# Optimization experiments

Measured on AMD Instinct MI355X. Metric: run time of the kernel, lower is better.

Reference implementation:

```python
import jax, jax.numpy as jnp
import numpy as np

B, N, E = 128, 256, 2048
BINS = 16

def _gcn(x, src, dst, W, b):
    # GCNConv with self-loops and symmetric deg^-1/2 normalization (PyG default).
    h = x @ W  # [N, Fout]
    deg = jnp.zeros(x.shape[0], x.dtype).at[dst].add(1.0) + 1.0  # +1 self-loop
    dinv = jax.lax.rsqrt(deg)
    coef = dinv[src] * dinv[dst]  # [E]
    agg = jnp.zeros_like(h).at[dst].add(h[src] * coef[:, None])
    return agg + h / deg[:, None] + b  # self-loop norm = 1/deg

def _gnn(x, ei, W1, b1, W2, b2, W3, b3):
    # x: [B,N,Fin], ei: [B,2,E]. Dropout skipped (eval mode).
    def single(x, ei):
        s, d = ei[0], ei[1]
        h = jax.nn.relu(_gcn(x, s, d, W1, b1))
        h = jax.nn.relu(_gcn(h, s, d, W2, b2))
        return _gcn(h, s, d, W3, b3)
    return jax.vmap(single)(x, ei)

def _att_pool(x, Watt):
    # SimGNN attention pooling; all graphs have exactly N nodes.
    ctx = jnp.tanh((x @ Watt.T).sum(axis=1) / jnp.asarray(N, x.dtype))  # [B,f3]
    scores = jax.nn.sigmoid(jnp.einsum('bnf,bf->bn', x, ctx))  # [B,N]
    return jnp.einsum('bnf,bn->bf', x, scores)  # [B,f3]

def _forward(xq, xc, eq, ec, W1, b1, W2, b2, W3, b3, Watt, ntnW, ntnV, ntnb, fc1W, fc1b, fc2W, fc2b):
    q = _gnn(xq, eq, W1, b1, W2, b2, W3, b3)  # [B,N,f3]
    c = _gnn(xc, ec, W1, b1, W2, b2, W3, b3)
    e1 = _att_pool(q, Watt)
    e2 = _att_pool(c, Watt)
    # NTN: bilinear + linear on concat + bias
    scores = jax.nn.relu(
        jnp.einsum('bi,tij,bj->bt', e1, ntnW, e2)
        + jnp.concatenate([e1, e2], axis=-1) @ ntnV.T
        + ntnb
    )  # [B, tensor_neurons]
    # histogram of all pairwise node-embedding dot products (torch.histc semantics)
    s = jnp.einsum('bnf,bmf->bnm', q, c).ravel()
    lo, hi = s.min(), s.max()
    idx = jnp.clip(jnp.floor((s - lo) / (hi - lo) * BINS).astype(jnp.int32), 0, BINS - 1)
    counts = jnp.zeros(BINS, s.dtype).at[idx].add(1.0)
    h = jax.lax.stop_gradient(counts / counts.sum())
    scores = jnp.concatenate([scores, jnp.broadcast_to(h, (scores.shape[0], BINS))], axis=1)
    scores = jax.nn.relu(scores @ fc1W.T + fc1b)
    p = jax.nn.sigmoid(scores @ fc2W.T + fc2b)  # [B,1]
    return p.squeeze()


def setup_inputs() -> dict:
    key = jax.random.key(0)
    ks = jax.random.split(key, 20)
    Fin, f1, f2, f3, T, BN = 128, 128, 64, 32, 16, 16
    def xav(k, shape):
        fan_in, fan_out = shape[-1], shape[0]
        lim = np.sqrt(6.0 / (fan_in + fan_out))
        return jax.random.uniform(k, shape, jnp.float32, -lim, lim)
    return {
        'xq': jax.random.normal(ks[0], (B, N, Fin), jnp.float32),
        'xc': jax.random.normal(ks[1], (B, N, Fin), jnp.float32),
        'eq': jax.random.randint(ks[2], (B, 2, E), 0, N, jnp.int32),
        'ec': jax.random.randint(ks[3], (B, 2, E), 0, N, jnp.int32),
        'W1': xav(ks[4], (Fin, f1)), 'b1': jnp.zeros((f1,), jnp.float32),
        'W2': xav(ks[5], (f1, f2)), 'b2': jnp.zeros((f2,), jnp.float32),
        'W3': xav(ks[6], (f2, f3)), 'b3': jnp.zeros((f3,), jnp.float32),
        'Watt': xav(ks[7], (f3, f3)),
        'ntnW': xav(ks[8], (T, f3, f3)),
        'ntnV': xav(ks[9], (T, 2 * f3)),
        'ntnb': xav(ks[10], (T, 1)).squeeze(-1),
        'fc1W': xav(ks[11], (BN, T + BINS)), 'fc1b': jnp.zeros((BN,), jnp.float32),
        'fc2W': xav(ks[12], (1, BN)), 'fc2b': jnp.zeros((1,), jnp.float32),
    }


def reference(xq, xc, eq, ec, W1, b1, W2, b2, W3, b3, Watt, ntnW, ntnV, ntnb, fc1W, fc1b, fc2W, fc2b):
    return _forward(xq, xc, eq, ec, W1, b1, W2, b2, W3, b3, Watt, ntnW, ntnV, ntnb, fc1W, fc1b, fc2W, fc2b)
```

## Files before the change

### kernel.cpp

```cpp
#include <hip/hip_runtime.h>
#include <math.h>

#define BB 128
#define NN 256
#define EE 2048
#define BINS 16
#define HTS 36

typedef unsigned short u16;

__global__ void csr_kernel(const int* __restrict__ eq, const int* __restrict__ ec,
                           int* __restrict__ off, u16* __restrict__ srcs,
                           float* __restrict__ dvsg) {
    int g = blockIdx.x;
    int b = g < BB ? g : g - BB;
    const int* ei = g < BB ? eq : ec;
    int t = threadIdx.x;
    __shared__ int cnt[NN];
    __shared__ int sa[NN], sb[NN];
    __shared__ int cursor[NN];
    cnt[t] = 0;
    __syncthreads();
    const int* src = ei + b * 2 * EE;
    const int* dst = src + EE;
    for (int e = t; e < EE; e += 256) atomicAdd(&cnt[dst[e]], 1);
    __syncthreads();
    dvsg[g * NN + t] = rsqrtf((float)cnt[t] + 1.0f);
    sa[t] = cnt[t];
    __syncthreads();
    int* pin = sa; int* pout = sb;
    for (int d = 1; d < NN; d <<= 1) {
        int v = pin[t];
        if (t >= d) v += pin[t - d];
        pout[t] = v;
        __syncthreads();
        int* tmp = pin; pin = pout; pout = tmp;
    }
    int excl = pin[t] - cnt[t];
    off[g * 257 + t] = excl;
    if (t == 255) off[g * 257 + 256] = EE;
    cursor[t] = excl;
    __syncthreads();
    for (int e = t; e < EE; e += 256) {
        int d = dst[e], s = src[e];
        int pos = atomicAdd(&cursor[d], 1);
        srcs[g * EE + pos] = (u16)s;
    }
}

template<int FIN, int FOUT, bool RELU, int NSPLIT>
__global__ __launch_bounds__(256, 3) void gcn_fused3(
        const float* __restrict__ X0, const float* __restrict__ X1,
        const float* __restrict__ W, const float* __restrict__ bias,
        const int* __restrict__ off, const u16* __restrict__ srcs,
        const float* __restrict__ dvsg, float* __restrict__ OUT) {
    constexpr int CHUNKS = FOUT / 32;
    int blk = blockIdx.x;
    int g = blk % (2 * BB);
    int rest = blk / (2 * BB);
    int cb = (rest % CHUNKS) * 32;
    int half = rest / CHUNKS;
    int t = threadIdx.x;

    __shared__ float hT[NN * HTS];
    __shared__ float xsT[8 * 260];
    __shared__ float wt[8 * 32];
    __shared__ int   eoff[NN + 1];
    __shared__ u16   esrc[EE];
    __shared__ float dvs_s[NN];

    const float* xg = (g < BB) ? (X0 + (size_t)g * NN * FIN)
                               : (X1 + (size_t)(g - BB) * NN * FIN);
    const int* o = off + g * 257;
    const u16* sr = srcs + (size_t)g * EE;

    for (int i = t; i < EE; i += 256) esrc[i] = sr[i];
    for (int i = t; i <= NN; i += 256) eoff[i] = o[i];
    dvs_s[t] = dvsg[g * NN + t];

    int l = t & 63;
    int wv = t >> 6;

    float acc[4][8];
#pragma unroll
    for (int i = 0; i < 4; i++)
#pragma unroll
        for (int j = 0; j < 8; j++) acc[i][j] = 0.f;

    const float* xr = xg + t * FIN;
    float4 va = *(const float4*)(xr);
    float4 vb = *(const float4*)(xr + 4);
    int wrow = t >> 5, wcol = t & 31;
    float wreg = W[wrow * FOUT + cb + wcol];

    for (int k0 = 0; k0 < FIN; k0 += 8) {
        xsT[0 * 260 + t] = va.x;
        xsT[1 * 260 + t] = va.y;
        xsT[2 * 260 + t] = va.z;
        xsT[3 * 260 + t] = va.w;
        xsT[4 * 260 + t] = vb.x;
        xsT[5 * 260 + t] = vb.y;
        xsT[6 * 260 + t] = vb.z;
        xsT[7 * 260 + t] = vb.w;
        wt[t] = wreg;
        __syncthreads();
        if (k0 + 8 < FIN) {
            va = *(const float4*)(xr + k0 + 8);
            vb = *(const float4*)(xr + k0 + 12);
            wreg = W[(k0 + 8 + wrow) * FOUT + cb + wcol];
        }
#pragma unroll
        for (int k = 0; k < 8; k++) {
            float4 xv = *(const float4*)&xsT[k * 260 + 4 * l];
            float4 wa = *(const float4*)&wt[k * 32 + 8 * wv];
            float4 wb = *(const float4*)&wt[k * 32 + 8 * wv + 4];
            float xq4[4] = {xv.x, xv.y, xv.z, xv.w};
            float wc8[8] = {wa.x, wa.y, wa.z, wa.w, wb.x, wb.y, wb.z, wb.w};
#pragma unroll
            for (int i = 0; i < 4; i++)
#pragma unroll
                for (int j = 0; j < 8; j++) acc[i][j] += xq4[i] * wc8[j];
        }
        __syncthreads();
    }
#pragma unroll
    for (int i = 0; i < 4; i++) {
        *(float4*)&hT[(4 * l + i) * HTS + 8 * wv] =
            make_float4(acc[i][0], acc[i][1], acc[i][2], acc[i][3]);
        *(float4*)&hT[(4 * l + i) * HTS + 8 * wv + 4] =
            make_float4(acc[i][4], acc[i][5], acc[i][6], acc[i][7]);
    }
    __syncthreads();

    int c = t & 31, ng = t >> 5;
    float bb_ = bias[cb + c];
    float* outp = OUT + (size_t)g * NN * FOUT;
    constexpr int NSEG = NN / NSPLIT;
    int nlo = half * NSEG, nhi = nlo + NSEG;
    for (int n = nlo + ng; n < nhi; n += 8) {
        int j0 = eoff[n], j1 = eoff[n + 1];
        float dn = dvs_s[n];
        float a = 0.f;
        int j = j0;
        for (; j + 1 < j1; j += 2) {
            int s0 = esrc[j], s1 = esrc[j + 1];
            float w0 = dvs_s[s0] * dn, w1 = dvs_s[s1] * dn;
            a += hT[s0 * HTS + c] * w0;
            a += hT[s1 * HTS + c] * w1;
        }
        if (j < j1) {
            int s0 = esrc[j];
            a += hT[s0 * HTS + c] * (dvs_s[s0] * dn);
        }
        float d0i = 1.0f / ((float)(j1 - j0) + 1.0f);
        float val = a + hT[n * HTS + c] * d0i + bb_;
        if (RELU) val = fmaxf(val, 0.f);
        outp[n * FOUT + cb + c] = val;
    }
}

__global__ void attpool_kernel(const float* __restrict__ X, const float* __restrict__ Watt,
                               float* __restrict__ e) {
    int g = blockIdx.x;
    int t = threadIdx.x;
    __shared__ float xs[NN * 33];
    __shared__ float red[256];
    __shared__ float mean_s[32], ctx_s[32], sc[NN];
    const float* x = X + (size_t)g * NN * 32;
    for (int i = t; i < NN * 32; i += 256) { int n = i >> 5, c = i & 31; xs[n * 33 + c] = x[i]; }
    __syncthreads();
    {
        int c = t & 31, p = t >> 5;
        float s = 0.f;
        for (int n = p * 32; n < (p + 1) * 32; n++) s += xs[n * 33 + c];
        red[t] = s;
    }
    __syncthreads();
    if (t < 32) {
        float m = 0.f;
        for (int p = 0; p < 8; p++) m += red[p * 32 + t];
        mean_s[t] = m / (float)NN;
    }
    __syncthreads();
    if (t < 32) {
        float a = 0.f;
        for (int f = 0; f < 32; f++) a += mean_s[f] * Watt[t * 32 + f];
        ctx_s[t] = tanhf(a);
    }
    __syncthreads();
    {
        float a = 0.f;
        for (int f = 0; f < 32; f++) a += xs[t * 33 + f] * ctx_s[f];
        sc[t] = 1.f / (1.f + expf(-a));
    }
    __syncthreads();
    {
        int c = t & 31, p = t >> 5;
        float s = 0.f;
        for (int n = p * 32; n < (p + 1) * 32; n++) s += xs[n * 33 + c] * sc[n];
        red[t] = s;
    }
    __syncthreads();
    if (t < 32) {
        float s = 0.f;
        for (int p = 0; p < 8; p++) s += red[p * 32 + t];
        e[g * 32 + t] = s;
    }
}

#define PD_STAGE_AND_DOT \
    int blk = blockIdx.x; \
    int b = blk >> 2; \
    int tq = (blk >> 1) & 1, tc = blk & 1; \
    __shared__ float qsT[32 * 132]; \
    __shared__ float csT[32 * 132]; \
    int t = threadIdx.x; \
    { \
        int n = t >> 1, f0 = (t & 1) * 16; \
        const float* qp = Q + ((size_t)b * NN + tq * 128 + n) * 32 + f0; \
        const float* cp = C + ((size_t)b * NN + tc * 128 + n) * 32 + f0; \
        float qa16[16], ca16[16]; \
        *(float4*)&qa16[0]  = *(const float4*)(qp); \
        *(float4*)&qa16[4]  = *(const float4*)(qp + 4); \
        *(float4*)&qa16[8]  = *(const float4*)(qp + 8); \
        *(float4*)&qa16[12] = *(const float4*)(qp + 12); \
        *(float4*)&ca16[0]  = *(const float4*)(cp); \
        *(float4*)&ca16[4]  = *(const float4*)(cp + 4); \
        *(float4*)&ca16[8]  = *(const float4*)(cp + 8); \
        *(float4*)&ca16[12] = *(const float4*)(cp + 12); \
        _Pragma("unroll") \
        for (int m = 0; m < 16; m++) { \
            qsT[(f0 + m) * 132 + n] = qa16[m]; \
            csT[(f0 + m) * 132 + n] = ca16[m]; \
        } \
    } \
    __syncthreads(); \
    int rg = (t >> 4) * 4, cg = (t & 15) * 4; \
    float acc[8][8]; \
    _Pragma("unroll") \
    for (int i = 0; i < 8; i++) \
        _Pragma("unroll") \
        for (int j = 0; j < 8; j++) acc[i][j] = 0.f; \
    _Pragma("unroll 2") \
    for (int f = 0; f < 32; f++) { \
        float4 qa = *(const float4*)&qsT[f * 132 + rg]; \
        float4 qb = *(const float4*)&qsT[f * 132 + 64 + rg]; \
        float4 ca = *(const float4*)&csT[f * 132 + cg]; \
        float4 cb = *(const float4*)&csT[f * 132 + 64 + cg]; \
        float qv[8] = {qa.x, qa.y, qa.z, qa.w, qb.x, qb.y, qb.z, qb.w}; \
        float cv[8] = {ca.x, ca.y, ca.z, ca.w, cb.x, cb.y, cb.z, cb.w}; \
        _Pragma("unroll") \
        for (int i = 0; i < 8; i++) \
            _Pragma("unroll") \
            for (int j = 0; j < 8; j++) acc[i][j] += qv[i] * cv[j]; \
    }

__global__ __launch_bounds__(256, 4) void pairdot_minmax(
        const float* __restrict__ Q, const float* __restrict__ C,
        float* __restrict__ bmin, float* __restrict__ bmax) {
    PD_STAGE_AND_DOT
    float lmin = acc[0][0], lmax = acc[0][0];
#pragma unroll
    for (int i = 0; i < 8; i++)
#pragma unroll
        for (int j = 0; j < 8; j++) {
            lmin = fminf(lmin, acc[i][j]);
            lmax = fmaxf(lmax, acc[i][j]);
        }
    __shared__ float rmin[256], rmax[256];
    rmin[t] = lmin; rmax[t] = lmax;
    __syncthreads();
    for (int s = 128; s > 0; s >>= 1) {
        if (t < s) { rmin[t] = fminf(rmin[t], rmin[t + s]); rmax[t] = fmaxf(rmax[t], rmax[t + s]); }
        __syncthreads();
    }
    if (t == 0) { bmin[blk] = rmin[0]; bmax[blk] = rmax[0]; }
}

__global__ void minmax_kernel(const float* __restrict__ bmin, const float* __restrict__ bmax,
                              float* __restrict__ lohi, float* __restrict__ counts) {
    __shared__ float rmin[256], rmax[256];
    int t = threadIdx.x;
    float lmin = 1e30f, lmax = -1e30f;
    for (int i = t; i < 512; i += 256) { lmin = fminf(lmin, bmin[i]); lmax = fmaxf(lmax, bmax[i]); }
    rmin[t] = lmin; rmax[t] = lmax;
    __syncthreads();
    for (int s = 128; s > 0; s >>= 1) {
        if (t < s) { rmin[t] = fminf(rmin[t], rmin[t + s]); rmax[t] = fmaxf(rmax[t], rmax[t + s]); }
        __syncthreads();
    }
    if (t == 0) { lohi[0] = rmin[0]; lohi[1] = rmax[0]; }
    if (t < BINS) counts[t] = 0.f;
}

__global__ __launch_bounds__(256, 4) void pairdot_hist(
        const float* __restrict__ Q, const float* __restrict__ C,
        const float* __restrict__ lohi, float* __restrict__ counts) {
    PD_STAGE_AND_DOT
    float lo = lohi[0], hi = lohi[1];
    float scale = (float)BINS / (hi - lo);
    int lane = t & 63;
    int cnt = 0;
#pragma unroll
    for (int i = 0; i < 8; i++)
#pragma unroll
        for (int j = 0; j < 8; j++) {
            int idx = (int)floorf((acc[i][j] - lo) * scale);
            idx = min(max(idx, 0), BINS - 1);
            unsigned long long b0 = __ballot((idx & 1) != 0);
            unsigned long long b1 = __ballot((idx & 2) != 0);
            unsigned long long b2 = __ballot((idx & 4) != 0);
            unsigned long long b3 = __ballot((idx & 8) != 0);
            unsigned long long msk = ((lane & 1) ? b0 : ~b0);
            msk &= ((lane & 2) ? b1 : ~b1);
            msk &= ((lane & 4) ? b2 : ~b2);
            msk &= ((lane & 8) ? b3 : ~b3);
            cnt += __popcll(msk);
        }
    __shared__ float wbins[4][BINS];
    int wave = t >> 6;
    if (lane < BINS) wbins[wave][lane] = (float)cnt;
    __syncthreads();
    if (t < BINS) {
        atomicAdd(&counts[t], wbins[0][t] + wbins[1][t] + wbins[2][t] + wbins[3][t]);
    }
}

__global__ void final_kernel(const float* __restrict__ e1, const float* __restrict__ e2,
                             const float* __restrict__ ntnW, const float* __restrict__ ntnV,
                             const float* __restrict__ ntnb, const float* __restrict__ counts,
                             const float* __restrict__ fc1W, const float* __restrict__ fc1b,
                             const float* __restrict__ fc2W, const float* __restrict__ fc2b,
                             float* __restrict__ out) {
    int b = blockIdx.x;
    int t = threadIdx.x;
    __shared__ float a1[32], a2[32], red[256], z[32], u[16];
    if (t < 32) a1[t] = e1[b * 32 + t];
    else if (t < 64) a2[t - 32] = e2[b * 32 + t - 32];
    __syncthreads();
    int tt = t >> 4, g = t & 15;
    float p = 0.f;
#pragma unroll
    for (int ii = 0; ii < 2; ii++) {
        int i = g + 16 * ii;
        float d = 0.f;
        const float* wr = ntnW + (tt * 32 + i) * 32;
        for (int j = 0; j < 32; j++) d += wr[j] * a2[j];
        p += a1[i] * d;
    }
    red[t] = p;
    __syncthreads();
    if (t < 16) {
        float s = 0.f;
        for (int g2 = 0; g2 < 16; g2++) s += red[t * 16 + g2];
        float lin = ntnb[t];
        for (int i = 0; i < 32; i++) lin += ntnV[t * 64 + i] * a1[i];
        for (int i = 0; i < 32; i++) lin += ntnV[t * 64 + 32 + i] * a2[i];
        z[t] = fmaxf(s + lin, 0.f);
    } else if (t < 32) {
        float tot = 0.f;
        for (int i = 0; i < BINS; i++) tot += counts[i];
        z[t] = counts[t - 16] / tot;
    }
    __syncthreads();
    if (t < 16) {
        float a = fc1b[t];
        for (int i = 0; i < 32; i++) a += fc1W[t * 32 + i] * z[i];
        u[t] = fmaxf(a, 0.f);
    }
    __syncthreads();
    if (t == 0) {
        float a = fc2b[0];
        for (int i = 0; i < 16; i++) a += fc2W[i] * u[i];
        out[b] = 1.f / (1.f + expf(-a));
    }
}

extern "C" void kernel_launch(void* const* d_in, const int* in_sizes, int n_in,
                              void* d_out, int out_size, void* d_ws, size_t ws_size,
                              hipStream_t stream) {
    const float* xq   = (const float*)d_in[0];
    const float* xc   = (const float*)d_in[1];
    const int*   eq   = (const int*)d_in[2];
    const int*   ec   = (const int*)d_in[3];
    const float* W1   = (const float*)d_in[4];
    const float* b1   = (const float*)d_in[5];
    const float* W2   = (const float*)d_in[6];
    const float* b2   = (const float*)d_in[7];
    const float* W3   = (const float*)d_in[8];
    const float* b3   = (const float*)d_in[9];
    const float* Watt = (const float*)d_in[10];
    const float* ntnW = (const float*)d_in[11];
    const float* ntnV = (const float*)d_in[12];
    const float* ntnb = (const float*)d_in[13];
    const float* fc1W = (const float*)d_in[14];
    const float* fc1b = (const float*)d_in[15];
    const float* fc2W = (const float*)d_in[16];
    const float* fc2b = (const float*)d_in[17];
    float* out = (float*)d_out;
    float* ws  = (float*)d_ws;

    float* O3   = ws;
    float* e12  = O3 + 2097152;
    float* bmin = e12 + 8192;
    float* bmax = bmin + 2048;
    float* lohi = bmax + 2048;
    float* cntw = lohi + 2;
    int*   off  = (int*)(ws + 2109504);
    u16*   srcs = (u16*)(off + 65792);
    float* dvsg = ws + 2109504 + 65792 + 524288;
    float* O1   = ws + 3223872;
    float* O2   = O1 + 8388608;

    float* O3Q = O3;
    float* O3C = O3 + (size_t)BB * NN * 32;
    float* e1w = e12;
    float* e2w = e12 + BB * 32;

    csr_kernel<<<2 * BB, 256, 0, stream>>>(eq, ec, off, srcs, dvsg);

    gcn_fused3<128, 128, true, 1><<<4 * 2 * BB, 256, 0, stream>>>(
        xq, xc, W1, b1, off, srcs, dvsg, O1);
    gcn_fused3<128, 64, true, 1><<<2 * 2 * BB, 256, 0, stream>>>(
        O1, O1 + (size_t)BB * NN * 128, W2, b2, off, srcs, dvsg, O2);
    gcn_fused3<64, 32, false, 2><<<2 * 2 * BB, 256, 0, stream>>>(
        O2, O2 + (size_t)BB * NN * 64, W3, b3, off, srcs, dvsg, O3);

    attpool_kernel<<<2 * BB, 256, 0, stream>>>(O3, Watt, e12);

    pairdot_minmax<<<BB * 4, 256, 0, stream>>>(O3Q, O3C, bmin, bmax);
    minmax_kernel<<<1, 256, 0, stream>>>(bmin, bmax, lohi, cntw);
    pairdot_hist<<<BB * 4, 256, 0, stream>>>(O3Q, O3C, lohi, cntw);

    final_kernel<<<BB, 256, 0, stream>>>(e1w, e2w, ntnW, ntnV, ntnb, cntw,
                                         fc1W, fc1b, fc2W, fc2b, out);
}
```

Measured before the change: 327.9 us.

## Split fused GCN layers into separate row-tiled GEMM and gather kernels

Each fused per-graph GCN kernel, which recomputed the GEMM per 32-column chunk with a small 8-wide K tile, is replaced by a standalone row-tiled GEMM kernel writing H to a workspace buffer, followed by a gather kernel that aggregates neighbours from H staged in shared memory. Layer 1 is split into two 64-column halves so one temporary buffer can be reused, and O2 aliases O1 to shrink the workspace. The goal is better GEMM tiling (K=16, full-width output tiles, higher occupancy) and less redundant X reading. The cost is extra global round trips of H and twice as many kernel launches.

```diff
diff --git a/kernel.cpp b/kernel.cpp
--- a/kernel.cpp
+++ b/kernel.cpp
@@ -5,7 +5,6 @@
 #define NN 256
 #define EE 2048
 #define BINS 16
-#define HTS 36
 
 typedef unsigned short u16;
 
@@ -48,114 +47,137 @@
     }
 }
 
-template<int FIN, int FOUT, bool RELU, int NSPLIT>
-__global__ __launch_bounds__(256, 3) void gcn_fused3(
+template<int FIN, int FOUT, int WLD>
+__global__ __launch_bounds__(256, 4) void gemm_k(
         const float* __restrict__ X0, const float* __restrict__ X1,
-        const float* __restrict__ W, const float* __restrict__ bias,
+        const float* __restrict__ W, float* __restrict__ H) {
+    constexpr int NCG = FOUT / 4;
+    constexpr int NRG = 256 / NCG;
+    constexpr int TILE_R = NRG * 4;
+    constexpr int XSTR = TILE_R + 4;
+    constexpr int NF4 = TILE_R / 64;
+    __shared__ float xsT[16 * XSTR];
+    __shared__ float wt[16 * FOUT];
+    int t = threadIdx.x;
+    size_t row0 = (size_t)blockIdx.x * TILE_R;
+
+    const float* xp[NF4];
+#pragma unroll
+    for (int i = 0; i < NF4; i++) {
+        int f = t + 256 * i;
+        int r = f >> 2;
+        size_t gr = row0 + r;
+        const float* base = (gr < (size_t)BB * NN)
+                            ? X0 + gr * FIN
+                            : X1 + (gr - (size_t)BB * NN) * FIN;
+        xp[i] = base + (f & 3) * 4;
+    }
+    float4 xa[NF4];
+#pragma unroll
+    for (int i = 0; i < NF4; i++) xa[i] = *(const float4*)xp[i];
+
+    int wrow, wcol; bool wact;
+    if (FOUT == 64) { wrow = t >> 4; wcol = (t & 15) * 4; wact = true; }
+    else            { wrow = t >> 3; wcol = (t & 7) * 4;  wact = (t < 128); }
+    float4 wa4 = make_float4(0.f, 0.f, 0.f, 0.f);
+    if (wact) wa4 = *(const float4*)&W[(size_t)wrow * WLD + wcol];
+
+    int colg = t & (NCG - 1); int cg = colg * 4;
+    int rowg = t / NCG;       int rg = rowg * 4;
+
+    float acc[4][4];
+#pragma unroll
+    for (int i = 0; i < 4; i++)
+#pragma unroll
+        for (int j = 0; j < 4; j++) acc[i][j] = 0.f;
+
+    for (int k0 = 0; k0 < FIN; k0 += 16) {
+#pragma unroll
+        for (int i = 0; i < NF4; i++) {
+            int f = t + 256 * i;
+            int r = f >> 2;
+            int kq = (f & 3) * 4;
+            xsT[(kq + 0) * XSTR + r] = xa[i].x;
+            xsT[(kq + 1) * XSTR + r] = xa[i].y;
+            xsT[(kq + 2) * XSTR + r] = xa[i].z;
+            xsT[(kq + 3) * XSTR + r] = xa[i].w;
+        }
+        if (wact) *(float4*)&wt[wrow * FOUT + wcol] = wa4;
+        __syncthreads();
+        if (k0 + 16 < FIN) {
+#pragma unroll
+            for (int i = 0; i < NF4; i++) xa[i] = *(const float4*)(xp[i] + k0 + 16);
+            if (wact) wa4 = *(const float4*)&W[(size_t)(k0 + 16 + wrow) * WLD + wcol];
+        }
+#pragma unroll
+        for (int k = 0; k < 16; k++) {
+            float4 xv = *(const float4*)&xsT[k * XSTR + rg];
+            float4 wv = *(const float4*)&wt[k * FOUT + cg];
+            acc[0][0] += xv.x * wv.x; acc[0][1] += xv.x * wv.y;
+            acc[0][2] += xv.x * wv.z; acc[0][3] += xv.x * wv.w;
+            acc[1][0] += xv.y * wv.x; acc[1][1] += xv.y * wv.y;
+            acc[1][2] += xv.y * wv.z; acc[1][3] += xv.y * wv.w;
+            acc[2][0] += xv.z * wv.x; acc[2][1] += xv.z * wv.y;
+            acc[2][2] += xv.z * wv.z; acc[2][3] += xv.z * wv.w;
+            acc[3][0] += xv.w * wv.x; acc[3][1] += xv.w * wv.y;
+            acc[3][2] += xv.w * wv.z; acc[3][3] += xv.w * wv.w;
+        }
+        __syncthreads();
+    }
+#pragma unroll
+    for (int i = 0; i < 4; i++) {
+        *(float4*)&H[(row0 + rg + i) * FOUT + cg] =
+            make_float4(acc[i][0], acc[i][1], acc[i][2], acc[i][3]);
+    }
+}
+
+template<int FH, int OLD, bool RELU>
+__global__ __launch_bounds__(256, 4) void gather_k(
+        const float* __restrict__ H, const float* __restrict__ bias,
         const int* __restrict__ off, const u16* __restrict__ srcs,
         const float* __restrict__ dvsg, float* __restrict__ OUT) {
-    constexpr int CHUNKS = FOUT / 32;
+    constexpr int NCH = FH / 32;
     int blk = blockIdx.x;
-    int g = blk % (2 * BB);
-    int rest = blk / (2 * BB);
-    int cb = (rest % CHUNKS) * 32;
-    int half = rest / CHUNKS;
-    int t = threadIdx.x;
-
-    __shared__ float hT[NN * HTS];
-    __shared__ float xsT[8 * 260];
-    __shared__ float wt[8 * 32];
+    int g = blk / NCH, ch = blk % NCH;
+    int cb = ch * 32;
+    __shared__ float hT[NN * 33];
     __shared__ int   eoff[NN + 1];
     __shared__ u16   esrc[EE];
     __shared__ float dvs_s[NN];
-
-    const float* xg = (g < BB) ? (X0 + (size_t)g * NN * FIN)
-                               : (X1 + (size_t)(g - BB) * NN * FIN);
+    int t = threadIdx.x;
+    const float* Hg = H + (size_t)g * NN * FH + cb;
+#pragma unroll
+    for (int i = 0; i < 8; i++) {
+        int idx = t + 256 * i;
+        int n = idx >> 3, c4 = (idx & 7) * 4;
+        float4 v = *(const float4*)&Hg[(size_t)n * FH + c4];
+        hT[n * 33 + c4 + 0] = v.x;
+        hT[n * 33 + c4 + 1] = v.y;
+        hT[n * 33 + c4 + 2] = v.z;
+        hT[n * 33 + c4 + 3] = v.w;
+    }
+    const u16* sr = srcs + (size_t)g * EE;
+    for (int i = t; i < EE; i += 256) esrc[i] = sr[i];
     const int* o = off + g * 257;
-    const u16* sr = srcs + (size_t)g * EE;
-
-    for (int i = t; i < EE; i += 256) esrc[i] = sr[i];
     for (int i = t; i <= NN; i += 256) eoff[i] = o[i];
     dvs_s[t] = dvsg[g * NN + t];
-
-    int l = t & 63;
-    int wv = t >> 6;
-
-    float acc[4][8];
-#pragma unroll
-    for (int i = 0; i < 4; i++)
-#pragma unroll
-        for (int j = 0; j < 8; j++) acc[i][j] = 0.f;
-
-    const float* xr = xg + t * FIN;
-    float4 va = *(const float4*)(xr);
-    float4 vb = *(const float4*)(xr + 4);
-    int wrow = t >> 5, wcol = t & 31;
-    float wreg = W[wrow * FOUT + cb + wcol];
-
-    for (int k0 = 0; k0 < FIN; k0 += 8) {
-        xsT[0 * 260 + t] = va.x;
-        xsT[1 * 260 + t] = va.y;
-        xsT[2 * 260 + t] = va.z;
-        xsT[3 * 260 + t] = va.w;
-        xsT[4 * 260 + t] = vb.x;
-        xsT[5 * 260 + t] = vb.y;
-        xsT[6 * 260 + t] = vb.z;
-        xsT[7 * 260 + t] = vb.w;
-        wt[t] = wreg;
-        __syncthreads();
-        if (k0 + 8 < FIN) {
-            va = *(const float4*)(xr + k0 + 8);
-            vb = *(const float4*)(xr + k0 + 12);
-            wreg = W[(k0 + 8 + wrow) * FOUT + cb + wcol];
-        }
-#pragma unroll
-        for (int k = 0; k < 8; k++) {
-            float4 xv = *(const float4*)&xsT[k * 260 + 4 * l];
-            float4 wa = *(const float4*)&wt[k * 32 + 8 * wv];
-            float4 wb = *(const float4*)&wt[k * 32 + 8 * wv + 4];
-            float xq4[4] = {xv.x, xv.y, xv.z, xv.w};
-            float wc8[8] = {wa.x, wa.y, wa.z, wa.w, wb.x, wb.y, wb.z, wb.w};
-#pragma unroll
-            for (int i = 0; i < 4; i++)
-#pragma unroll
-                for (int j = 0; j < 8; j++) acc[i][j] += xq4[i] * wc8[j];
-        }
-        __syncthreads();
-    }
-#pragma unroll
-    for (int i = 0; i < 4; i++) {
-        *(float4*)&hT[(4 * l + i) * HTS + 8 * wv] =
-            make_float4(acc[i][0], acc[i][1], acc[i][2], acc[i][3]);
-        *(float4*)&hT[(4 * l + i) * HTS + 8 * wv + 4] =
-            make_float4(acc[i][4], acc[i][5], acc[i][6], acc[i][7]);
-    }
     __syncthreads();
 
     int c = t & 31, ng = t >> 5;
     float bb_ = bias[cb + c];
-    float* outp = OUT + (size_t)g * NN * FOUT;
-    constexpr int NSEG = NN / NSPLIT;
-    int nlo = half * NSEG, nhi = nlo + NSEG;
-    for (int n = nlo + ng; n < nhi; n += 8) {
+    float* outp = OUT + (size_t)g * NN * OLD + cb + c;
+    for (int n = ng; n < NN; n += 8) {
         int j0 = eoff[n], j1 = eoff[n + 1];
         float dn = dvs_s[n];
         float a = 0.f;
-        int j = j0;
-        for (; j + 1 < j1; j += 2) {
-            int s0 = esrc[j], s1 = esrc[j + 1];
-            float w0 = dvs_s[s0] * dn, w1 = dvs_s[s1] * dn;
-            a += hT[s0 * HTS + c] * w0;
-            a += hT[s1 * HTS + c] * w1;
-        }
-        if (j < j1) {
-            int s0 = esrc[j];
-            a += hT[s0 * HTS + c] * (dvs_s[s0] * dn);
+        for (int j = j0; j < j1; j++) {
+            int s = esrc[j];
+            a += hT[s * 33 + c] * (dvs_s[s] * dn);
         }
         float d0i = 1.0f / ((float)(j1 - j0) + 1.0f);
-        float val = a + hT[n * HTS + c] * d0i + bb_;
+        float val = a + hT[n * 33 + c] * d0i + bb_;
         if (RELU) val = fmaxf(val, 0.f);
-        outp[n * FOUT + cb + c] = val;
+        outp[(size_t)n * OLD] = val;
     }
 }
 
@@ -408,9 +430,10 @@
     float* cntw = lohi + 2;
     int*   off  = (int*)(ws + 2109504);
     u16*   srcs = (u16*)(off + 65792);
-    float* dvsg = ws + 2109504 + 65792 + 524288;
-    float* O1   = ws + 3223872;
-    float* O2   = O1 + 8388608;
+    float* dvsg = ws + 2437440;
+    float* Htmp = ws + 2502976;
+    float* O1   = ws + 6697280;
+    float* O2   = O1;
 
     float* O3Q = O3;
     float* O3C = O3 + (size_t)BB * NN * 32;
@@ -419,12 +442,16 @@
 
     csr_kernel<<<2 * BB, 256, 0, stream>>>(eq, ec, off, srcs, dvsg);
 
-    gcn_fused3<128, 128, true, 1><<<4 * 2 * BB, 256, 0, stream>>>(
-        xq, xc, W1, b1, off, srcs, dvsg, O1);
-    gcn_fused3<128, 64, true, 1><<<2 * 2 * BB, 256, 0, stream>>>(
-        O1, O1 + (size_t)BB * NN * 128, W2, b2, off, srcs, dvsg, O2);
-    gcn_fused3<64, 32, false, 2><<<2 * 2 * BB, 256, 0, stream>>>(
-        O2, O2 + (size_t)BB * NN * 64, W3, b3, off, srcs, dvsg, O3);
+    gemm_k<128, 64, 128><<<1024, 256, 0, stream>>>(xq, xc, W1, Htmp);
+    gather_k<64, 128, true><<<512, 256, 0, stream>>>(Htmp, b1, off, srcs, dvsg, O1);
+    gemm_k<128, 64, 128><<<1024, 256, 0, stream>>>(xq, xc, W1 + 64, Htmp);
+    gather_k<64, 128, true><<<512, 256, 0, stream>>>(Htmp, b1 + 64, off, srcs, dvsg, O1 + 64);
+
+    gemm_k<128, 64, 64><<<1024, 256, 0, stream>>>(O1, O1 + (size_t)BB * NN * 128, W2, Htmp);
+    gather_k<64, 64, true><<<512, 256, 0, stream>>>(Htmp, b2, off, srcs, dvsg, O2);
+
+    gemm_k<64, 32, 32><<<512, 256, 0, stream>>>(O2, O2 + (size_t)BB * NN * 64, W3, Htmp);
+    gather_k<32, 32, false><<<256, 256, 0, stream>>>(Htmp, b3, off, srcs, dvsg, O3);
 
     attpool_kernel<<<2 * BB, 256, 0, stream>>>(O3, Watt, e12);
 
```

Result: slower. 547.8 us (+67.1%).

## Widen GCN blocks to 512 threads with aliased shared buffer and smaller tiles

Applied to the files above, without the earlier changes.

The fused GCN kernel now runs 512 threads per block, and each thread computes a 4x4 output tile instead of 4x8. The k-step grows from 8 to 16, and the aggregation loop strides over 16 node groups. The staging buffers for X and W share one shared-memory array with the h tile, which shrinks LDS use so more blocks can be resident. The intent is higher occupancy and fewer register-heavy accumulators, traded against less register reuse per FMA and the change in LDS padding from 36 to 33, which drops float4 stores and may cause bank conflicts.

```diff
diff --git a/kernel.cpp b/kernel.cpp
--- a/kernel.cpp
+++ b/kernel.cpp
@@ -5,7 +5,6 @@
 #define NN 256
 #define EE 2048
 #define BINS 16
-#define HTS 36
 
 typedef unsigned short u16;
 
@@ -49,7 +48,7 @@
 }
 
 template<int FIN, int FOUT, bool RELU, int NSPLIT>
-__global__ __launch_bounds__(256, 3) void gcn_fused3(
+__global__ __launch_bounds__(512, 8) void gcn_fused4(
         const float* __restrict__ X0, const float* __restrict__ X1,
         const float* __restrict__ W, const float* __restrict__ bias,
         const int* __restrict__ off, const u16* __restrict__ srcs,
@@ -62,74 +61,75 @@
     int half = rest / CHUNKS;
     int t = threadIdx.x;
 
-    __shared__ float hT[NN * HTS];
-    __shared__ float xsT[8 * 260];
-    __shared__ float wt[8 * 32];
+    __shared__ float uni[NN * 33];
     __shared__ int   eoff[NN + 1];
     __shared__ u16   esrc[EE];
     __shared__ float dvs_s[NN];
+    float* xsT = uni;
+    float* wt  = uni + 16 * 260;
+    float* hT  = uni;
 
     const float* xg = (g < BB) ? (X0 + (size_t)g * NN * FIN)
                                : (X1 + (size_t)(g - BB) * NN * FIN);
     const int* o = off + g * 257;
     const u16* sr = srcs + (size_t)g * EE;
 
-    for (int i = t; i < EE; i += 256) esrc[i] = sr[i];
-    for (int i = t; i <= NN; i += 256) eoff[i] = o[i];
-    dvs_s[t] = dvsg[g * NN + t];
+    for (int i = t; i < EE; i += 512) esrc[i] = sr[i];
+    for (int i = t; i <= NN; i += 512) eoff[i] = o[i];
+    if (t < NN) dvs_s[t] = dvsg[g * NN + t];
 
     int l = t & 63;
     int wv = t >> 6;
 
-    float acc[4][8];
+    float acc[4][4];
 #pragma unroll
     for (int i = 0; i < 4; i++)
 #pragma unroll
-        for (int j = 0; j < 8; j++) acc[i][j] = 0.f;
-
-    const float* xr = xg + t * FIN;
-    float4 va = *(const float4*)(xr);
-    float4 vb = *(const float4*)(xr + 4);
-    int wrow = t >> 5, wcol = t & 31;
-    float wreg = W[wrow * FOUT + cb + wcol];
-
-    for (int k0 = 0; k0 < FIN; k0 += 8) {
-        xsT[0 * 260 + t] = va.x;
-        xsT[1 * 260 + t] = va.y;
-        xsT[2 * 260 + t] = va.z;
-        xsT[3 * 260 + t] = va.w;
-        xsT[4 * 260 + t] = vb.x;
-        xsT[5 * 260 + t] = vb.y;
-        xsT[6 * 260 + t] = vb.z;
-        xsT[7 * 260 + t] = vb.w;
+        for (int j = 0; j < 4; j++) acc[i][j] = 0.f;
+
+    int sn = t >> 1, qk = (t & 1) * 8;
+    const float* xr = xg + sn * FIN + qk;
+    float4 v0 = *(const float4*)xr;
+    float4 v1 = *(const float4*)(xr + 4);
+    float wreg = W[(t >> 5) * FOUT + cb + (t & 31)];
+
+    for (int k0 = 0; k0 < FIN; k0 += 16) {
+        xsT[(qk + 0) * 260 + sn] = v0.x;
+        xsT[(qk + 1) * 260 + sn] = v0.y;
+        xsT[(qk + 2) * 260 + sn] = v0.z;
+        xsT[(qk + 3) * 260 + sn] = v0.w;
+        xsT[(qk + 4) * 260 + sn] = v1.x;
+        xsT[(qk + 5) * 260 + sn] = v1.y;
+        xsT[(qk + 6) * 260 + sn] = v1.z;
+        xsT[(qk + 7) * 260 + sn] = v1.w;
         wt[t] = wreg;
         __syncthreads();
-        if (k0 + 8 < FIN) {
-            va = *(const float4*)(xr + k0 + 8);
-            vb = *(const float4*)(xr + k0 + 12);
-            wreg = W[(k0 + 8 + wrow) * FOUT + cb + wcol];
-        }
-#pragma unroll
-        for (int k = 0; k < 8; k++) {
+        if (k0 + 16 < FIN) {
+            xr += 16;
+            v0 = *(const float4*)xr;
+            v1 = *(const float4*)(xr + 4);
+            wreg = W[(k0 + 16 + (t >> 5)) * FOUT + cb + (t & 31)];
+        }
+#pragma unroll
+        for (int k = 0; k < 16; k++) {
             float4 xv = *(const float4*)&xsT[k * 260 + 4 * l];
-            float4 wa = *(const float4*)&wt[k * 32 + 8 * wv];
-            float4 wb = *(const float4*)&wt[k * 32 + 8 * wv + 4];
-            float xq4[4] = {xv.x, xv.y, xv.z, xv.w};
-            float wc8[8] = {wa.x, wa.y, wa.z, wa.w, wb.x, wb.y, wb.z, wb.w};
-#pragma unroll
-            for (int i = 0; i < 4; i++)
-#pragma unroll
-                for (int j = 0; j < 8; j++) acc[i][j] += xq4[i] * wc8[j];
+            float4 wvv = *(const float4*)&wt[k * 32 + 4 * wv];
+            acc[0][0] += xv.x * wvv.x; acc[0][1] += xv.x * wvv.y;
+            acc[0][2] += xv.x * wvv.z; acc[0][3] += xv.x * wvv.w;
+            acc[1][0] += xv.y * wvv.x; acc[1][1] += xv.y * wvv.y;
+            acc[1][2] += xv.y * wvv.z; acc[1][3] += xv.y * wvv.w;
+            acc[2][0] += xv.z * wvv.x; acc[2][1] += xv.z * wvv.y;
+            acc[2][2] += xv.z * wvv.z; acc[2][3] += xv.z * wvv.w;
+            acc[3][0] += xv.w * wvv.x; acc[3][1] += xv.w * wvv.y;
+            acc[3][2] += xv.w * wvv.z; acc[3][3] += xv.w * wvv.w;
         }
         __syncthreads();
     }
 #pragma unroll
-    for (int i = 0; i < 4; i++) {
-        *(float4*)&hT[(4 * l + i) * HTS + 8 * wv] =
-            make_float4(acc[i][0], acc[i][1], acc[i][2], acc[i][3]);
-        *(float4*)&hT[(4 * l + i) * HTS + 8 * wv + 4] =
-            make_float4(acc[i][4], acc[i][5], acc[i][6], acc[i][7]);
-    }
+    for (int i = 0; i < 4; i++)
+#pragma unroll
+        for (int j = 0; j < 4; j++)
+            hT[(4 * l + i) * 33 + 4 * wv + j] = acc[i][j];
     __syncthreads();
 
     int c = t & 31, ng = t >> 5;
@@ -137,23 +137,22 @@
     float* outp = OUT + (size_t)g * NN * FOUT;
     constexpr int NSEG = NN / NSPLIT;
     int nlo = half * NSEG, nhi = nlo + NSEG;
-    for (int n = nlo + ng; n < nhi; n += 8) {
+    for (int n = nlo + ng; n < nhi; n += 16) {
         int j0 = eoff[n], j1 = eoff[n + 1];
         float dn = dvs_s[n];
         float a = 0.f;
         int j = j0;
         for (; j + 1 < j1; j += 2) {
             int s0 = esrc[j], s1 = esrc[j + 1];
-            float w0 = dvs_s[s0] * dn, w1 = dvs_s[s1] * dn;
-            a += hT[s0 * HTS + c] * w0;
-            a += hT[s1 * HTS + c] * w1;
+            a += hT[s0 * 33 + c] * (dvs_s[s0] * dn);
+            a += hT[s1 * 33 + c] * (dvs_s[s1] * dn);
         }
         if (j < j1) {
             int s0 = esrc[j];
-            a += hT[s0 * HTS + c] * (dvs_s[s0] * dn);
+            a += hT[s0 * 33 + c] * (dvs_s[s0] * dn);
         }
         float d0i = 1.0f / ((float)(j1 - j0) + 1.0f);
-        float val = a + hT[n * HTS + c] * d0i + bb_;
+        float val = a + hT[n * 33 + c] * d0i + bb_;
         if (RELU) val = fmaxf(val, 0.f);
         outp[n * FOUT + cb + c] = val;
     }
@@ -408,7 +407,7 @@
     float* cntw = lohi + 2;
     int*   off  = (int*)(ws + 2109504);
     u16*   srcs = (u16*)(off + 65792);
-    float* dvsg = ws + 2109504 + 65792 + 524288;
+    float* dvsg = ws + 2437440;
     float* O1   = ws + 3223872;
     float* O2   = O1 + 8388608;
 
@@ -419,11 +418,11 @@
 
     csr_kernel<<<2 * BB, 256, 0, stream>>>(eq, ec, off, srcs, dvsg);
 
-    gcn_fused3<128, 128, true, 1><<<4 * 2 * BB, 256, 0, stream>>>(
+    gcn_fused4<128, 128, true, 1><<<4 * 2 * BB, 512, 0, stream>>>(
         xq, xc, W1, b1, off, srcs, dvsg, O1);
-    gcn_fused3<128, 64, true, 1><<<2 * 2 * BB, 256, 0, stream>>>(
+    gcn_fused4<128, 64, true, 1><<<2 * 2 * BB, 512, 0, stream>>>(
         O1, O1 + (size_t)BB * NN * 128, W2, b2, off, srcs, dvsg, O2);
-    gcn_fused3<64, 32, false, 2><<<2 * 2 * BB, 256, 0, stream>>>(
+    gcn_fused4<64, 32, false, 2><<<2 * 2 * BB, 512, 0, stream>>>(
         O2, O2 + (size_t)BB * NN * 64, W3, b3, off, srcs, dvsg, O3);
 
     attpool_kernel<<<2 * BB, 256, 0, stream>>>(O3, Watt, e12);
```

After: 367.4 us. 12.1% more time.
